# Optimization experiments

Measured on AMD Instinct MI355X. Metric: run time of the kernel, lower is better.

Reference implementation:

```python
import jax, jax.numpy as jnp
import numpy as np

H = 50  # LSTM units
T = 10  # NUMBARS
F = 5   # input features
B = 131072


def _lstm(x, W, U, b):
    """Keras-default LSTM. x: [B,T,Fin], W: [Fin,4H], U: [H,4H], b: [4H].
    Gate order i,f,g(c),o; sigmoid recurrent act, tanh cell act, zero init state.
    Returns (all_h [B,T,H], last_h [B,H])."""
    Bn = x.shape[0]
    h0 = jnp.zeros((Bn, H), x.dtype)
    c0 = jnp.zeros((Bn, H), x.dtype)

    def step(carry, xt):
        h, c = carry
        z = xt @ W + h @ U + b  # [B,4H]
        i, f, g, o = jnp.split(z, 4, axis=-1)
        i = jax.nn.sigmoid(i)
        f = jax.nn.sigmoid(f)
        g = jnp.tanh(g)
        o = jax.nn.sigmoid(o)
        c_new = f * c + i * g
        h_new = o * jnp.tanh(c_new)
        return (h_new, c_new), h_new

    (h_last, _), hs = jax.lax.scan(step, (h0, c0), jnp.swapaxes(x, 0, 1))
    return jnp.swapaxes(hs, 0, 1), h_last


def setup_inputs() -> dict:
    key = jax.random.key(0)
    ks = jax.random.split(key, 16)
    d = {"x": jax.random.normal(ks[0], (B, T, F), dtype=jnp.float32)}
    in_dims = [F, H, H, H]
    for l in range(4):
        s_in = 1.0 / np.sqrt(in_dims[l])
        s_h = 1.0 / np.sqrt(H)
        d[f"W{l+1}"] = jax.random.normal(ks[1 + 3 * l], (in_dims[l], 4 * H), dtype=jnp.float32) * s_in
        d[f"U{l+1}"] = jax.random.normal(ks[2 + 3 * l], (H, 4 * H), dtype=jnp.float32) * s_h
        # Keras unit_forget_bias: forget-gate bias = 1
        b = jnp.zeros((4 * H,), jnp.float32).at[H:2 * H].set(1.0)
        d[f"b{l+1}"] = b
    d["Wd1"] = jax.random.normal(ks[13], (H, 50), dtype=jnp.float32) * (1.0 / np.sqrt(H))
    d["bd1"] = jnp.zeros((50,), jnp.float32)
    d["Wd2"] = jax.random.normal(ks[14], (50, 1), dtype=jnp.float32) * (1.0 / np.sqrt(50))
    d["bd2"] = jnp.zeros((1,), jnp.float32)
    return d


def reference(x, W1, U1, b1, W2, U2, b2, W3, U3, b3, W4, U4, b4, Wd1, bd1, Wd2, bd2):
    # Dropout layers are identity at inference (Keras default training=False).
    h, _ = _lstm(x, W1, U1, b1)
    h, _ = _lstm(h, W2, U2, b2)
    h, _ = _lstm(h, W3, U3, b3)
    _, h = _lstm(h, W4, U4, b4)        # return_sequences=False -> last h [B,H]
    h = h @ Wd1 + bd1                   # Dense(50), linear activation
    out = jax.nn.sigmoid(h @ Wd2 + bd2) # Dense(1, sigmoid) -> [B,1]
    return out
```

## Files before the change

kernel.cpp:

```cpp
#include <hip/hip_runtime.h>


typedef __attribute__((ext_vector_type(8))) short short8;
typedef __attribute__((ext_vector_type(4))) float floatx4;
typedef __attribute__((ext_vector_type(2))) float float2v;
typedef unsigned short u16;
typedef unsigned int u32;

constexpr int H_ = 50, T_ = 10, F_ = 5;
constexpr int MTILE = 32;
constexpr int BLKT = 256;
constexpr float LOG2E = 1.4426950408889634f;

__device__ __forceinline__ float rcp_(float x) { return __builtin_amdgcn_rcpf(x); }
__device__ __forceinline__ float exp2_(float x) { return __builtin_amdgcn_exp2f(x); }
__device__ __forceinline__ float sig_nat(float x) {
  return rcp_(1.0f + exp2_(-LOG2E * x));
}

__device__ __forceinline__ u16 f2bf(float f) {
  union { float f; unsigned u; } v; v.f = f;
  unsigned r = v.u + 0x7FFFu + ((v.u >> 16) & 1u);
  return (u16)(r >> 16);
}
__device__ __forceinline__ float bf2f(u16 s) {
  union { unsigned u; float f; } v; v.u = ((unsigned)s) << 16;
  return v.f;
}
__device__ __forceinline__ unsigned pk_bf16(float a, float b) {
  return (unsigned)f2bf(a) | ((unsigned)f2bf(b) << 16);
}

__global__ void prep_kernel(
    const float* W1, const float* U1, const float* b1, const float* W2,
    const float* U2, const float* b2, const float* W3, const float* U3,
    const float* b3, const float* W4, const float* U4, const float* b4,
    const float* Wd1, const float* bd1, const float* Wd2, const float* bd2,
    u16* Wpp, float* biasP, float* vdense) {
  int idx = blockIdx.x * blockDim.x + threadIdx.x;
  const float* Wt[4] = {W1, W2, W3, W4};
  const float* Ut[4] = {U1, U2, U3, U4};
  const float* bt[4] = {b1, b2, b3, b4};
  const int fin[4] = {F_, H_, H_, H_};
  if (idx < 4 * 32768) {
    int l = idx >> 15, r = idx & 32767;
    int j = r & 7, lane = (r >> 3) & 63, w = (r >> 9) & 3, gI = (r >> 11) & 3,
        kt = r >> 13;
    int row = kt * 32 + (lane >> 4) * 8 + j;
    int u = w * 16 + (lane & 15);
    float val = 0.0f;
    if (u < H_) {
      if (row < 64) {
        if (row < fin[l]) val = Wt[l][row * 200 + gI * H_ + u];
      } else {
        int rr = row - 64;
        if (rr < H_) val = Ut[l][rr * 200 + gI * H_ + u];
      }
    }
    val *= (gI == 2) ? (2.0f * LOG2E) : (-LOG2E);
    Wpp[idx] = f2bf(val);
  } else if (idx < 4 * 32768 + 1024) {
    int r = idx - 4 * 32768;
    int l = r >> 8, q = r & 255, gI = q >> 6, u = q & 63;
    float val = (u < H_) ? bt[l][gI * H_ + u] : 0.0f;
    biasP[r] = val * ((gI == 2) ? (2.0f * LOG2E) : (-LOG2E));
  } else if (idx < 4 * 32768 + 1024 + 51) {
    int u = idx - (4 * 32768 + 1024);
    if (u < H_) {
      float s = 0.0f;
      for (int n = 0; n < H_; ++n) s += Wd1[u * H_ + n] * Wd2[n];
      vdense[u] = s;
    } else {
      float s = bd2[0];
      for (int n = 0; n < H_; ++n) s += bd1[n] * Wd2[n];
      vdense[50] = s;
    }
  }
}

__global__ __launch_bounds__(BLKT, 3) void lstm_fused(
    const float* __restrict__ x0, const u16* __restrict__ Wpp,
    const float* __restrict__ biasP, const float* __restrict__ vdense,
    float* __restrict__ out) {
  __shared__ __align__(16) u16 buf[T_ * 2048];
  __shared__ __align__(16) u16 xb[T_ * 256];
  __shared__ __align__(16) u16 zc[8];

  const int tid = threadIdx.x;
  const int w = tid >> 6, lane = tid & 63;
  const int np = lane & 15, quad = lane >> 4;
  const int b0 = blockIdx.x * MTILE;
  const int u = w * 16 + np;

  for (int i = tid; i < T_ * 128; i += BLKT) ((u32*)xb)[i] = 0;
  if (tid < 4) ((u32*)zc)[tid] = 0;
  __syncthreads();

  for (int e = tid; e < MTILE * 50; e += BLKT) {
    int row = e / 50, q = e - row * 50;
    int t = q / 5, f = q - t * 5;
    xb[t * 256 + row * 8 + f] = f2bf(x0[(size_t)(b0 + row) * 50 + q]);
  }
  __syncthreads();

  const int rbase = quad * 128 + np * 8;
  const int cb0 = (w >> 1) * 512 + ((w & 1) * 2 + (np >> 3)) * 128 + quad * 32 + (np & 7);

  float2v cst[4];

#pragma unroll 1
  for (int l = 0; l < 4; ++l) {
    const u16* wp = Wpp + l * 32768;
    short8 bfr[4][4];
#pragma unroll
    for (int kt = 0; kt < 4; ++kt)
#pragma unroll
      for (int g = 0; g < 4; ++g)
        bfr[kt][g] = *(const short8*)&wp[(((kt * 4 + g) * 4 + w) * 64 + lane) * 8];
    float bv[4];
#pragma unroll
    for (int g = 0; g < 4; ++g) bv[g] = biasP[l * 256 + g * 64 + u];
#pragma unroll
    for (int i = 0; i < 4; ++i) cst[i] = float2v{0.0f, 0.0f};

#pragma unroll 1
    for (int t = 0; t < T_; ++t) {
      u16* bt = &buf[t * 2048];
      const u16* bp = &buf[(t == 0 ? 0 : (t - 1)) * 2048];

      floatx4 acc[2][4];
#pragma unroll
      for (int mt = 0; mt < 2; ++mt)
#pragma unroll
        for (int g = 0; g < 4; ++g)
          acc[mt][g] = floatx4{bv[g], bv[g], bv[g], bv[g]};

      if (l == 0) {
#pragma unroll
        for (int mt = 0; mt < 2; ++mt) {
          const u16* ap = (quad == 0) ? &xb[t * 256 + (mt * 16 + np) * 8] : zc;
          short8 af = *(const short8*)ap;
#pragma unroll
          for (int g = 0; g < 4; ++g)
            acc[mt][g] = __builtin_amdgcn_mfma_f32_16x16x32_bf16(
                af, bfr[0][g], acc[mt][g], 0, 0, 0);
        }
      } else {
#pragma unroll
        for (int mt = 0; mt < 2; ++mt) {
          short8 a0 = *(const short8*)&bt[mt * 1024 + rbase];
          short8 a1 = *(const short8*)&bt[mt * 1024 + 512 + rbase];
#pragma unroll
          for (int g = 0; g < 4; ++g) {
            acc[mt][g] = __builtin_amdgcn_mfma_f32_16x16x32_bf16(
                a0, bfr[0][g], acc[mt][g], 0, 0, 0);
            acc[mt][g] = __builtin_amdgcn_mfma_f32_16x16x32_bf16(
                a1, bfr[1][g], acc[mt][g], 0, 0, 0);
          }
        }
      }
      if (t > 0) {
#pragma unroll
        for (int mt = 0; mt < 2; ++mt) {
          short8 h0 = *(const short8*)&bp[mt * 1024 + rbase];
          short8 h1 = *(const short8*)&bp[mt * 1024 + 512 + rbase];
#pragma unroll
          for (int g = 0; g < 4; ++g) {
            acc[mt][g] = __builtin_amdgcn_mfma_f32_16x16x32_bf16(
                h0, bfr[2][g], acc[mt][g], 0, 0, 0);
            acc[mt][g] = __builtin_amdgcn_mfma_f32_16x16x32_bf16(
                h1, bfr[3][g], acc[mt][g], 0, 0, 0);
          }
        }
      }
      if (l > 0) __syncthreads();

#pragma unroll
      for (int mt = 0; mt < 2; ++mt) {
#pragma unroll
        for (int p = 0; p < 2; ++p) {
          float2v di = {exp2_(acc[mt][0][2 * p]), exp2_(acc[mt][0][2 * p + 1])};
          float2v df = {exp2_(acc[mt][1][2 * p]), exp2_(acc[mt][1][2 * p + 1])};
          float2v dg = {exp2_(acc[mt][2][2 * p]), exp2_(acc[mt][2][2 * p + 1])};
          float2v do_ = {exp2_(acc[mt][3][2 * p]), exp2_(acc[mt][3][2 * p + 1])};
          di += 1.0f; df += 1.0f; dg += 1.0f; do_ += 1.0f;
          float2v m1 = di * df, m2 = do_ * dg;
          float2v P = m1 * m2;
          float Rs = rcp_(P.x * P.y);
          float2v R = {Rs * P.y, Rs * P.x};
          float2v i_ = (df * m2) * R;
          float2v f_ = (di * m2) * R;
          float2v o_ = (m1 * dg) * R;
          float2v g_ = 1.0f - 2.0f * ((m1 * do_) * R);
          float2v cn = f_ * cst[mt * 2 + p] + i_ * g_;
          cst[mt * 2 + p] = cn;
          float2v s = cn * (2.0f * LOG2E);
          float2v dc = {exp2_(s.x), exp2_(s.y)};
          dc += 1.0f;
          float Rc = rcp_(dc.x * dc.y);
          float2v tc = 1.0f - 2.0f * float2v{Rc * dc.y, Rc * dc.x};
          float2v h = o_ * tc;
          unsigned pk = pk_bf16(h.x, h.y);
          int a0 = cb0 + mt * 1024 + p * 16;
          bt[a0] = (u16)pk;
          bt[a0 + 8] = (u16)(pk >> 16);
        }
      }
      __syncthreads();
    }
  }

  if (tid < MTILE) {
    int mt = tid >> 4, rr = tid & 15;
    const u16* b9 = &buf[9 * 2048];
    float s = vdense[50];
    for (int k = 0; k < H_; ++k) {
      int kk = k >> 5, qd = (k & 31) >> 3, j = k & 7;
      s += bf2f(b9[mt * 1024 + kk * 512 + qd * 128 + rr * 8 + j]) * vdense[k];
    }
    out[b0 + tid] = sig_nat(s);
  }
}

extern "C" void kernel_launch(void* const* d_in, const int* in_sizes, int n_in,
                              void* d_out, int out_size, void* d_ws,
                              size_t ws_size, hipStream_t stream) {
  const float* x = (const float*)d_in[0];
  const float* W1 = (const float*)d_in[1];
  const float* U1 = (const float*)d_in[2];
  const float* b1 = (const float*)d_in[3];
  const float* W2 = (const float*)d_in[4];
  const float* U2 = (const float*)d_in[5];
  const float* b2 = (const float*)d_in[6];
  const float* W3 = (const float*)d_in[7];
  const float* U3 = (const float*)d_in[8];
  const float* b3 = (const float*)d_in[9];
  const float* W4 = (const float*)d_in[10];
  const float* U4 = (const float*)d_in[11];
  const float* b4 = (const float*)d_in[12];
  const float* Wd1 = (const float*)d_in[13];
  const float* bd1 = (const float*)d_in[14];
  const float* Wd2 = (const float*)d_in[15];
  const float* bd2 = (const float*)d_in[16];

  const int Bn = in_sizes[0] / (T_ * F_);
  const int nblk = Bn / MTILE;
  char* ws = (char*)d_ws;
  u16* Wpp = (u16*)ws;
  float* biasP = (float*)(ws + 262144);
  float* vdense = (float*)(ws + 262144 + 4096);
  float* out = (float*)d_out;

  prep_kernel<<<(4 * 32768 + 1024 + 51 + 255) / 256, 256, 0, stream>>>(
      W1, U1, b1, W2, U2, b2, W3, U3, b3, W4, U4, b4, Wd1, bd1, Wd2, bd2, Wpp,
      biasP, vdense);

  lstm_fused<<<dim3(nblk), dim3(BLKT), 0, stream>>>(x, Wpp, biasP, vdense, out);
}
```

Measured before the change: 487.9 us.

## Reuse sequence buffer for layer-0 input, raise occupancy, use hardware bf16 pack

Layer-0 inputs are now staged directly into the shared sequence buffer in the layout later layers read, so the separate xb/zc LDS arrays and the special layer-0 path go away and all layers share one MFMA code path. That path needs a barrier every step, including layer 0. Launch bounds are raised from 3 to 4 blocks per SM so more blocks can be resident, at the risk of register spilling. The software round-to-nearest bf16 conversion is replaced by the v_cvt_pk_bf16_f32 instruction to cut ALU work in the gate epilogue.

```diff
diff --git a/kernel.cpp b/kernel.cpp
--- a/kernel.cpp
+++ b/kernel.cpp
@@ -27,8 +27,10 @@
   union { unsigned u; float f; } v; v.u = ((unsigned)s) << 16;
   return v.f;
 }
-__device__ __forceinline__ unsigned pk_bf16(float a, float b) {
-  return (unsigned)f2bf(a) | ((unsigned)f2bf(b) << 16);
+__device__ __forceinline__ unsigned cvt_pk_bf16(float lo, float hi) {
+  unsigned r;
+  asm("v_cvt_pk_bf16_f32 %0, %1, %2" : "=v"(r) : "v"(lo), "v"(hi));
+  return r;
 }
 
 __global__ void prep_kernel(
@@ -78,13 +80,11 @@
   }
 }
 
-__global__ __launch_bounds__(BLKT, 3) void lstm_fused(
+__global__ __launch_bounds__(BLKT, 4) void lstm_fused(
     const float* __restrict__ x0, const u16* __restrict__ Wpp,
     const float* __restrict__ biasP, const float* __restrict__ vdense,
     float* __restrict__ out) {
   __shared__ __align__(16) u16 buf[T_ * 2048];
-  __shared__ __align__(16) u16 xb[T_ * 256];
-  __shared__ __align__(16) u16 zc[8];
 
   const int tid = threadIdx.x;
   const int w = tid >> 6, lane = tid & 63;
@@ -92,14 +92,13 @@
   const int b0 = blockIdx.x * MTILE;
   const int u = w * 16 + np;
 
-  for (int i = tid; i < T_ * 128; i += BLKT) ((u32*)xb)[i] = 0;
-  if (tid < 4) ((u32*)zc)[tid] = 0;
+  for (int i = tid; i < T_ * 1024; i += BLKT) ((u32*)buf)[i] = 0;
   __syncthreads();
-
   for (int e = tid; e < MTILE * 50; e += BLKT) {
     int row = e / 50, q = e - row * 50;
     int t = q / 5, f = q - t * 5;
-    xb[t * 256 + row * 8 + f] = f2bf(x0[(size_t)(b0 + row) * 50 + q]);
+    buf[t * 2048 + (row >> 4) * 1024 + (row & 15) * 8 + f] =
+        f2bf(x0[(size_t)(b0 + row) * 50 + q]);
   }
   __syncthreads();
 
@@ -135,28 +134,19 @@
         for (int g = 0; g < 4; ++g)
           acc[mt][g] = floatx4{bv[g], bv[g], bv[g], bv[g]};
 
-      if (l == 0) {
-#pragma unroll
-        for (int mt = 0; mt < 2; ++mt) {
-          const u16* ap = (quad == 0) ? &xb[t * 256 + (mt * 16 + np) * 8] : zc;
-          short8 af = *(const short8*)ap;
+#pragma unroll
+      for (int mt = 0; mt < 2; ++mt) {
+        short8 a0 = *(const short8*)&bt[mt * 1024 + rbase];
+#pragma unroll
+        for (int g = 0; g < 4; ++g)
+          acc[mt][g] = __builtin_amdgcn_mfma_f32_16x16x32_bf16(
+              a0, bfr[0][g], acc[mt][g], 0, 0, 0);
+        if (l > 0) {
+          short8 a1 = *(const short8*)&bt[mt * 1024 + 512 + rbase];
 #pragma unroll
           for (int g = 0; g < 4; ++g)
             acc[mt][g] = __builtin_amdgcn_mfma_f32_16x16x32_bf16(
-                af, bfr[0][g], acc[mt][g], 0, 0, 0);
-        }
-      } else {
-#pragma unroll
-        for (int mt = 0; mt < 2; ++mt) {
-          short8 a0 = *(const short8*)&bt[mt * 1024 + rbase];
-          short8 a1 = *(const short8*)&bt[mt * 1024 + 512 + rbase];
-#pragma unroll
-          for (int g = 0; g < 4; ++g) {
-            acc[mt][g] = __builtin_amdgcn_mfma_f32_16x16x32_bf16(
-                a0, bfr[0][g], acc[mt][g], 0, 0, 0);
-            acc[mt][g] = __builtin_amdgcn_mfma_f32_16x16x32_bf16(
                 a1, bfr[1][g], acc[mt][g], 0, 0, 0);
-          }
         }
       }
       if (t > 0) {
@@ -173,7 +163,7 @@
           }
         }
       }
-      if (l > 0) __syncthreads();
+      __syncthreads();
 
 #pragma unroll
       for (int mt = 0; mt < 2; ++mt) {
@@ -200,7 +190,7 @@
           float Rc = rcp_(dc.x * dc.y);
           float2v tc = 1.0f - 2.0f * float2v{Rc * dc.y, Rc * dc.x};
           float2v h = o_ * tc;
-          unsigned pk = pk_bf16(h.x, h.y);
+          unsigned pk = cvt_pk_bf16(h.x, h.y);
           int a0 = cb0 + mt * 1024 + p * 16;
           bt[a0] = (u16)pk;
           bt[a0 + 8] = (u16)(pk >> 16);
```

Result: no change. 491.9 us (+0.8%).
